# Kernel tuning notes

Hardware: AMD Instinct MI355X
Metric: run time of the kernel (lower is better)

Reference implementation:

```python
import jax, jax.numpy as jnp
import numpy as np

# Paul Kellet pink-noise filter coefficients (verbatim from the torch source)
_A = np.array([0.99886, 0.99332, 0.969, 0.8665, 0.55, -0.7616], dtype=np.float32)   # pole feedback
_C = np.array([0.0555179, 0.0750759, 0.153852, 0.3104856, 0.5329522, -0.016898], dtype=np.float32)  # input gains
_B6_GAIN = 0.115926   # b6 is the previous white sample scaled (one-sample delay)
_DIRECT = 0.5362      # direct white feedthrough
_OUT_GAIN = 0.11


def setup_inputs() -> dict:
    key = jax.random.key(0)
    B, L = 256, 65536
    white = jax.random.normal(key, (B, L), dtype=jnp.float32)
    return {"white": white}


def reference(white):
    """Pink noise via the 6-pole IIR recurrence from SignalGenerator.noise('pink'),
    vectorized over a batch of channels; sequential time handled by lax.scan.
    white: [B, L] -> pink: [B, L]
    """
    B, L = white.shape
    a = jnp.asarray(_A)  # [6]
    c = jnp.asarray(_C)  # [6]

    def step(carry, w_t):
        # carry: (b [B,6] pole states, b6 [B] delayed-white state); w_t: [B]
        b, b6 = carry
        b = a * b + w_t[:, None] * c                      # [B,6]
        pink_t = (b.sum(-1) + b6 + _DIRECT * w_t) * _OUT_GAIN  # [B]
        return (b, _B6_GAIN * w_t), pink_t

    init = (jnp.zeros((B, 6), dtype=white.dtype), jnp.zeros((B,), dtype=white.dtype))
    _, pink_tb = jax.lax.scan(step, init, white.T)  # scan over time: [L, B]
    return pink_tb.T  # [B, L]
```

## Files before the change

### kernel.cpp

```cpp
#include <hip/hip_runtime.h>


constexpr int kL = 65536;
constexpr int kTile = 4096;
constexpr int kThr = 256;
constexpr int kChunk = 16;
constexpr int kTilesPerCh = kL / kTile;

__device__ __forceinline__ int swz(int i) {
    return i ^ (((i >> 5) & 7) << 2);
}

__global__ __launch_bounds__(kThr) void pink_tile_totals(
    const float* __restrict__ white, float* __restrict__ tile_e, int nTiles)
{
    constexpr float A[6] = {0.99886f, 0.99332f, 0.969f, 0.8665f, 0.55f, -0.7616f};
    constexpr float C[6] = {0.0555179f, 0.0750759f, 0.153852f, 0.3104856f, 0.5329522f, -0.016898f};

    __shared__ __align__(16) float buf[kTile];
    __shared__ float ssum[6][4];

    const int tid = threadIdx.x, lane = tid & 63, wave = tid >> 6;
    const int blk = blockIdx.x;

    const float4* src = (const float4*)(white + (size_t)blk * kTile);
    float4 v[4];
    #pragma unroll
    for (int k = 0; k < 4; ++k) v[k] = src[tid + k * kThr];
    #pragma unroll
    for (int k = 0; k < 4; ++k)
        *(float4*)&buf[swz(4 * (tid + k * kThr))] = v[k];

    float pmR[6];
    #pragma unroll
    for (int p = 0; p < 6; ++p) {
        float q = A[p];
        #pragma unroll
        for (int i = 0; i < 4; ++i) q *= q;
        float pm = 1.f;
        const int r = 255 - tid;
        #pragma unroll
        for (int b = 0; b < 8; ++b) { if ((r >> b) & 1) pm *= q; q *= q; }
        pmR[p] = pm;
    }
    __syncthreads();

    float w[kChunk];
    #pragma unroll
    for (int kk = 0; kk < kChunk / 4; ++kk) {
        float4 x = *(const float4*)&buf[swz(kChunk * tid + 4 * kk)];
        w[4*kk] = x.x; w[4*kk+1] = x.y; w[4*kk+2] = x.z; w[4*kk+3] = x.w;
    }

    float e[6] = {0.f, 0.f, 0.f, 0.f, 0.f, 0.f};
    #pragma unroll
    for (int k = 0; k < kChunk; ++k) {
        const float ww = w[k];
        #pragma unroll
        for (int p = 0; p < 6; ++p) e[p] = fmaf(A[p], e[p], ww * C[p]);
    }
    #pragma unroll
    for (int p = 0; p < 6; ++p) e[p] *= pmR[p];

    #pragma unroll
    for (int m = 1; m < 64; m <<= 1) {
        #pragma unroll
        for (int p = 0; p < 6; ++p) e[p] += __shfl_xor(e[p], m);
    }
    if (lane == 0) {
        #pragma unroll
        for (int p = 0; p < 6; ++p) ssum[p][wave] = e[p];
    }
    __syncthreads();
    if (tid < 6)
        tile_e[(size_t)tid * nTiles + blk] =
            ssum[tid][0] + ssum[tid][1] + ssum[tid][2] + ssum[tid][3];
}

__global__ __launch_bounds__(256) void pink_tile_prefix(
    const float* __restrict__ tile_e, float* __restrict__ tile_P, int nTiles)
{
    constexpr float A[6] = {0.99886f, 0.99332f, 0.969f, 0.8665f, 0.55f, -0.7616f};
    const int p  = blockIdx.x;
    const int ch = blockIdx.y * 256 + threadIdx.x;
    const int nCh = nTiles / kTilesPerCh;
    if (ch >= nCh) return;

    float Mt = A[p];
    #pragma unroll
    for (int i = 0; i < 12; ++i) Mt *= Mt;

    const float* ep = tile_e + (size_t)p * nTiles + (size_t)ch * kTilesPerCh;
    float*       Pp = tile_P + (size_t)p * nTiles + (size_t)ch * kTilesPerCh;
    float P = 0.f;
    #pragma unroll
    for (int t = 0; t < kTilesPerCh; ++t) {
        Pp[t] = P;
        P = fmaf(Mt, P, ep[t]);
    }
}

__global__ __launch_bounds__(kThr) void pink_outputs(
    const float* __restrict__ white, const float* __restrict__ tile_P,
    float* __restrict__ pink, int nTiles)
{
    constexpr float A[6] = {0.99886f, 0.99332f, 0.969f, 0.8665f, 0.55f, -0.7616f};
    constexpr float C[6] = {0.0555179f, 0.0750759f, 0.153852f, 0.3104856f, 0.5329522f, -0.016898f};
    constexpr float B6G = 0.115926f, DIRECT = 0.5362f, OUTG = 0.11f;

    __shared__ __align__(16) float buf[kTile];
    __shared__ float swv[6][4];

    const int tid = threadIdx.x, lane = tid & 63, wave = tid >> 6;
    const int blk = blockIdx.x;
    const size_t base = (size_t)blk * kTile;

    float P[6];
    #pragma unroll
    for (int p = 0; p < 6; ++p) P[p] = tile_P[(size_t)p * nTiles + blk];

    float pw0 = 0.f;
    if (tid == 0 && (blk & (kTilesPerCh - 1)) != 0) pw0 = white[base - 1];

    const float4* src = (const float4*)(white + base);
    float4 v[4];
    #pragma unroll
    for (int k = 0; k < 4; ++k) v[k] = src[tid + k * kThr];
    #pragma unroll
    for (int k = 0; k < 4; ++k)
        *(float4*)&buf[swz(4 * (tid + k * kThr))] = v[k];

    float m16[6], pmL[6], Mwv[6];
    #pragma unroll
    for (int p = 0; p < 6; ++p) {
        float q = A[p];
        #pragma unroll
        for (int i = 0; i < 4; ++i) q *= q;
        m16[p] = q;
        float pm = 1.f, qq = q;
        #pragma unroll
        for (int b = 0; b < 6; ++b) { if ((lane >> b) & 1) pm *= qq; qq *= qq; }
        pmL[p] = pm;
        Mwv[p] = qq;
    }
    __syncthreads();

    float w[kChunk];
    #pragma unroll
    for (int kk = 0; kk < kChunk / 4; ++kk) {
        float4 x = *(const float4*)&buf[swz(kChunk * tid + 4 * kk)];
        w[4*kk] = x.x; w[4*kk+1] = x.y; w[4*kk+2] = x.z; w[4*kk+3] = x.w;
    }
    const float pwl = (tid == 0) ? pw0 : buf[swz(kChunk * tid - 1)];

    float e[6] = {0.f, 0.f, 0.f, 0.f, 0.f, 0.f};
    #pragma unroll
    for (int k = 0; k < kChunk; ++k) {
        const float ww = w[k];
        #pragma unroll
        for (int p = 0; p < 6; ++p) e[p] = fmaf(A[p], e[p], ww * C[p]);
    }

    float mk[6];
    #pragma unroll
    for (int p = 0; p < 6; ++p) mk[p] = m16[p];
    #pragma unroll
    for (int r = 0; r < 6; ++r) {
        const int off = 1 << r;
        float fe[6];
        #pragma unroll
        for (int p = 0; p < 6; ++p) fe[p] = __shfl_up(e[p], off);
        if (lane >= off) {
            #pragma unroll
            for (int p = 0; p < 6; ++p) e[p] = fmaf(mk[p], fe[p], e[p]);
        }
        #pragma unroll
        for (int p = 0; p < 6; ++p) mk[p] *= mk[p];
    }
    float ex[6];
    #pragma unroll
    for (int p = 0; p < 6; ++p) {
        ex[p] = __shfl_up(e[p], 1);
        if (lane == 0) ex[p] = 0.f;
    }
    if (lane == 63) {
        #pragma unroll
        for (int p = 0; p < 6; ++p) swv[p][wave] = e[p];
    }
    __syncthreads();

    float b[6];
    #pragma unroll
    for (int p = 0; p < 6; ++p) {
        float X = P[p];
        #pragma unroll
        for (int w2 = 0; w2 < 3; ++w2)
            if (w2 < wave) X = fmaf(Mwv[p], X, swv[p][w2]);
        b[p] = fmaf(pmL[p], X, ex[p]);
    }
    float b6 = B6G * pwl;

    #pragma unroll
    for (int kk = 0; kk < kChunk / 4; ++kk) {
        float4 o;
        float* op = &o.x;
        #pragma unroll
        for (int j = 0; j < 4; ++j) {
            const float ww = w[4*kk + j];
            #pragma unroll
            for (int p = 0; p < 6; ++p) b[p] = fmaf(A[p], b[p], ww * C[p]);
            const float sum = ((b[0]+b[1]) + (b[2]+b[3])) + ((b[4]+b[5]) + b6);
            op[j] = fmaf(DIRECT, ww, sum) * OUTG;
            b6 = B6G * ww;
        }
        *(float4*)&buf[swz(kChunk * tid + 4 * kk)] = o;
    }
    __syncthreads();

    float4* dst = (float4*)(pink + base);
    #pragma unroll
    for (int k = 0; k < 4; ++k)
        dst[tid + k * kThr] = *(const float4*)&buf[swz(4 * (tid + k * kThr))];
}

extern "C" void kernel_launch(void* const* d_in, const int* in_sizes, int n_in,
                              void* d_out, int out_size, void* d_ws, size_t ws_size,
                              hipStream_t stream) {
    const float* white = (const float*)d_in[0];
    float* pink = (float*)d_out;
    const int nTiles = in_sizes[0] / kTile;
    const int nCh = nTiles / kTilesPerCh;
    float* tile_e = (float*)d_ws;
    float* tile_P = tile_e + (size_t)6 * nTiles;

    hipLaunchKernelGGL(pink_tile_totals, dim3(nTiles), dim3(kThr), 0, stream,
                       white, tile_e, nTiles);
    hipLaunchKernelGGL(pink_tile_prefix, dim3(6, (nCh + 255) / 256), dim3(256),
                       0, stream, tile_e, tile_P, nTiles);
    hipLaunchKernelGGL(pink_outputs, dim3(nTiles), dim3(kThr), 0, stream,
                       white, tile_P, pink, nTiles);
}
```

Measured before the change: 126.6 us.

## Fuse three-pass scan into single-pass decoupled lookback kernel

Replaces the totals, prefix and output kernels with one fused kernel. Each block takes a dynamic ticket, publishes its tile's aggregate with a release flag, then walks back over earlier tiles in its channel, accumulating their decayed aggregates until the decay factor becomes negligible. White noise is now read once instead of twice and two launches are removed. In exchange it adds a memset, spin-waiting on flags, and a truncated lookback whose accuracy depends on the pole decay.

```diff
diff --git a/kernel.cpp b/kernel.cpp
--- a/kernel.cpp
+++ b/kernel.cpp
@@ -11,98 +11,10 @@
     return i ^ (((i >> 5) & 7) << 2);
 }
 
-__global__ __launch_bounds__(kThr) void pink_tile_totals(
-    const float* __restrict__ white, float* __restrict__ tile_e, int nTiles)
-{
-    constexpr float A[6] = {0.99886f, 0.99332f, 0.969f, 0.8665f, 0.55f, -0.7616f};
-    constexpr float C[6] = {0.0555179f, 0.0750759f, 0.153852f, 0.3104856f, 0.5329522f, -0.016898f};
-
-    __shared__ __align__(16) float buf[kTile];
-    __shared__ float ssum[6][4];
-
-    const int tid = threadIdx.x, lane = tid & 63, wave = tid >> 6;
-    const int blk = blockIdx.x;
-
-    const float4* src = (const float4*)(white + (size_t)blk * kTile);
-    float4 v[4];
-    #pragma unroll
-    for (int k = 0; k < 4; ++k) v[k] = src[tid + k * kThr];
-    #pragma unroll
-    for (int k = 0; k < 4; ++k)
-        *(float4*)&buf[swz(4 * (tid + k * kThr))] = v[k];
-
-    float pmR[6];
-    #pragma unroll
-    for (int p = 0; p < 6; ++p) {
-        float q = A[p];
-        #pragma unroll
-        for (int i = 0; i < 4; ++i) q *= q;
-        float pm = 1.f;
-        const int r = 255 - tid;
-        #pragma unroll
-        for (int b = 0; b < 8; ++b) { if ((r >> b) & 1) pm *= q; q *= q; }
-        pmR[p] = pm;
-    }
-    __syncthreads();
-
-    float w[kChunk];
-    #pragma unroll
-    for (int kk = 0; kk < kChunk / 4; ++kk) {
-        float4 x = *(const float4*)&buf[swz(kChunk * tid + 4 * kk)];
-        w[4*kk] = x.x; w[4*kk+1] = x.y; w[4*kk+2] = x.z; w[4*kk+3] = x.w;
-    }
-
-    float e[6] = {0.f, 0.f, 0.f, 0.f, 0.f, 0.f};
-    #pragma unroll
-    for (int k = 0; k < kChunk; ++k) {
-        const float ww = w[k];
-        #pragma unroll
-        for (int p = 0; p < 6; ++p) e[p] = fmaf(A[p], e[p], ww * C[p]);
-    }
-    #pragma unroll
-    for (int p = 0; p < 6; ++p) e[p] *= pmR[p];
-
-    #pragma unroll
-    for (int m = 1; m < 64; m <<= 1) {
-        #pragma unroll
-        for (int p = 0; p < 6; ++p) e[p] += __shfl_xor(e[p], m);
-    }
-    if (lane == 0) {
-        #pragma unroll
-        for (int p = 0; p < 6; ++p) ssum[p][wave] = e[p];
-    }
-    __syncthreads();
-    if (tid < 6)
-        tile_e[(size_t)tid * nTiles + blk] =
-            ssum[tid][0] + ssum[tid][1] + ssum[tid][2] + ssum[tid][3];
-}
-
-__global__ __launch_bounds__(256) void pink_tile_prefix(
-    const float* __restrict__ tile_e, float* __restrict__ tile_P, int nTiles)
-{
-    constexpr float A[6] = {0.99886f, 0.99332f, 0.969f, 0.8665f, 0.55f, -0.7616f};
-    const int p  = blockIdx.x;
-    const int ch = blockIdx.y * 256 + threadIdx.x;
-    const int nCh = nTiles / kTilesPerCh;
-    if (ch >= nCh) return;
-
-    float Mt = A[p];
-    #pragma unroll
-    for (int i = 0; i < 12; ++i) Mt *= Mt;
-
-    const float* ep = tile_e + (size_t)p * nTiles + (size_t)ch * kTilesPerCh;
-    float*       Pp = tile_P + (size_t)p * nTiles + (size_t)ch * kTilesPerCh;
-    float P = 0.f;
-    #pragma unroll
-    for (int t = 0; t < kTilesPerCh; ++t) {
-        Pp[t] = P;
-        P = fmaf(Mt, P, ep[t]);
-    }
-}
-
-__global__ __launch_bounds__(kThr) void pink_outputs(
-    const float* __restrict__ white, const float* __restrict__ tile_P,
-    float* __restrict__ pink, int nTiles)
+__global__ __launch_bounds__(kThr) void pink_fused(
+    const float* __restrict__ white, float* __restrict__ pink,
+    unsigned int* __restrict__ ticket, unsigned int* __restrict__ flags,
+    float* __restrict__ tile_e, int nTiles)
 {
     constexpr float A[6] = {0.99886f, 0.99332f, 0.969f, 0.8665f, 0.55f, -0.7616f};
     constexpr float C[6] = {0.0555179f, 0.0750759f, 0.153852f, 0.3104856f, 0.5329522f, -0.016898f};
@@ -110,17 +22,15 @@
 
     __shared__ __align__(16) float buf[kTile];
     __shared__ float swv[6][4];
+    __shared__ float sP[6];
+    __shared__ unsigned int svb;
 
     const int tid = threadIdx.x, lane = tid & 63, wave = tid >> 6;
-    const int blk = blockIdx.x;
+
+    if (tid == 0) svb = atomicAdd(ticket, 1u);
+    __syncthreads();
+    const int blk = (int)svb;
     const size_t base = (size_t)blk * kTile;
-
-    float P[6];
-    #pragma unroll
-    for (int p = 0; p < 6; ++p) P[p] = tile_P[(size_t)p * nTiles + blk];
-
-    float pw0 = 0.f;
-    if (tid == 0 && (blk & (kTilesPerCh - 1)) != 0) pw0 = white[base - 1];
 
     const float4* src = (const float4*)(white + base);
     float4 v[4];
@@ -129,6 +39,9 @@
     #pragma unroll
     for (int k = 0; k < 4; ++k)
         *(float4*)&buf[swz(4 * (tid + k * kThr))] = v[k];
+
+    float pw0 = 0.f;
+    if (tid == 0 && (blk & (kTilesPerCh - 1)) != 0) pw0 = white[base - 1];
 
     float m16[6], pmL[6], Mwv[6];
     #pragma unroll
@@ -189,10 +102,48 @@
     }
     __syncthreads();
 
+    if (tid == 0) {
+        #pragma unroll
+        for (int p = 0; p < 6; ++p) {
+            float t = swv[p][0];
+            #pragma unroll
+            for (int w2 = 1; w2 < 4; ++w2) t = fmaf(Mwv[p], t, swv[p][w2]);
+            tile_e[(size_t)p * nTiles + blk] = t;
+        }
+        __hip_atomic_store(&flags[blk], 1u, __ATOMIC_RELEASE,
+                           __HIP_MEMORY_SCOPE_AGENT);
+
+        float Pl[6] = {0.f, 0.f, 0.f, 0.f, 0.f, 0.f};
+        const int tW = blk & (kTilesPerCh - 1);
+        if (tW) {
+            float A4k[6], cm[6];
+            #pragma unroll
+            for (int p = 0; p < 6; ++p) {
+                float q = Mwv[p] * Mwv[p]; q *= q;
+                A4k[p] = q; cm[p] = 1.f;
+            }
+            for (int s = tW - 1; s >= 0; --s) {
+                const int sb = (blk - tW) + s;
+                while (__hip_atomic_load(&flags[sb], __ATOMIC_ACQUIRE,
+                                         __HIP_MEMORY_SCOPE_AGENT) == 0u)
+                    __builtin_amdgcn_s_sleep(1);
+                #pragma unroll
+                for (int p = 0; p < 6; ++p) {
+                    Pl[p] = fmaf(cm[p], tile_e[(size_t)p * nTiles + sb], Pl[p]);
+                    cm[p] *= A4k[p];
+                }
+                if (cm[0] < 1e-12f) break;
+            }
+        }
+        #pragma unroll
+        for (int p = 0; p < 6; ++p) sP[p] = Pl[p];
+    }
+    __syncthreads();
+
     float b[6];
     #pragma unroll
     for (int p = 0; p < 6; ++p) {
-        float X = P[p];
+        float X = sP[p];
         #pragma unroll
         for (int w2 = 0; w2 < 3; ++w2)
             if (w2 < wave) X = fmaf(Mwv[p], X, swv[p][w2]);
@@ -229,14 +180,13 @@
     const float* white = (const float*)d_in[0];
     float* pink = (float*)d_out;
     const int nTiles = in_sizes[0] / kTile;
-    const int nCh = nTiles / kTilesPerCh;
-    float* tile_e = (float*)d_ws;
-    float* tile_P = tile_e + (size_t)6 * nTiles;
 
-    hipLaunchKernelGGL(pink_tile_totals, dim3(nTiles), dim3(kThr), 0, stream,
-                       white, tile_e, nTiles);
-    hipLaunchKernelGGL(pink_tile_prefix, dim3(6, (nCh + 255) / 256), dim3(256),
-                       0, stream, tile_e, tile_P, nTiles);
-    hipLaunchKernelGGL(pink_outputs, dim3(nTiles), dim3(kThr), 0, stream,
-                       white, tile_P, pink, nTiles);
+    unsigned int* ticket = (unsigned int*)d_ws;
+    unsigned int* flags  = ticket + 4;
+    float* tile_e = (float*)(flags + nTiles);
+
+    hipMemsetAsync(d_ws, 0, 16 + sizeof(unsigned int) * (size_t)nTiles, stream);
+
+    hipLaunchKernelGGL(pink_fused, dim3(nTiles), dim3(kThr), 0, stream,
+                       white, pink, ticket, flags, tile_e, nTiles);
 }
```

Measured after the change: 385.0 us. +204.0%, slower.
